# Kernel tuning notes

Hardware: AMD Instinct MI355X
Metric: run time of the kernel (lower is better)

The kernel has to match this reference:

```python
import jax, jax.numpy as jnp
import numpy as np

N = 65536      # samples
DX = 1024      # X features
DY = 1024      # Y features
D = 256        # projected width (x_net/y_net output)
LAMX = 0.1
LAMY = 0.1
SIGMA = 0.5    # STG gate noise std (eval-mode deterministic gate)
EPS = 0.001    # regularizer used in original code


def setup_inputs() -> dict:
    key = jax.random.key(0)
    ks = jax.random.split(key, 8)
    X = jax.random.normal(ks[0], (N, DX), dtype=jnp.float32)
    Y = jax.random.normal(ks[1], (N, DY), dtype=jnp.float32)
    # StochasticGates params (mu per input feature)
    mu_x = 0.01 * jax.random.normal(ks[2], (DX,), dtype=jnp.float32)
    mu_y = 0.01 * jax.random.normal(ks[3], (DY,), dtype=jnp.float32)
    # per-view linear nets (x_net: DX->D, y_net: DY->D)
    Wx = jax.random.normal(ks[4], (DX, D), dtype=jnp.float32) / np.sqrt(DX)
    bx = jnp.zeros((D,), dtype=jnp.float32)
    Wy = jax.random.normal(ks[5], (DY, D), dtype=jnp.float32) / np.sqrt(DY)
    by = jnp.zeros((D,), dtype=jnp.float32)
    return {"X": X, "Y": Y, "mu_x": mu_x, "mu_y": mu_y,
            "Wx": Wx, "bx": bx, "Wy": Wy, "by": by}


def _stg_gate(mu):
    # deterministic (eval) hard gate: clamp(mu + 0.5, 0, 1)
    return jnp.clip(mu + 0.5, 0.0, 1.0)


def _stg_reg(mu, lam):
    # lam * mean(P(gate > 0)) = lam * mean(Phi(mu/sigma))  [Gaussian CDF]
    return lam * jnp.mean(0.5 * (1.0 + jax.lax.erf(mu / (SIGMA * jnp.sqrt(2.0)))))


def _cov(a, b):
    # matches torch: (b.T @ a).T / (N-1) == a.T @ b / (N-1)
    n = a.shape[0]
    return (a.T @ b) / (n - 1)


def _inv_sqrt_sym(A):
    # A^(-1/2) via eigendecomposition; A symmetric so eigh == eig with V^-1 = V.T
    w, V = jnp.linalg.eigh(A)
    return (V * (w + EPS) ** (-0.5)) @ V.T


def _corr(Xh, Yh):
    d = Xh.shape[1]
    psi_x = Xh - Xh.mean(axis=0)
    psi_y = Yh - Yh.mean(axis=0)
    C_yy = _cov(psi_y, psi_y)
    C_yx = _cov(psi_y, psi_x)
    C_xy = _cov(psi_x, psi_y)
    C_xx = _cov(psi_x, psi_x)
    I = jnp.eye(d, dtype=Xh.dtype)
    C_yy_inv_root = _inv_sqrt_sym(C_yy + EPS * I)
    C_xx_inv = jnp.linalg.inv(C_xx + EPS * I)
    M = C_yy_inv_root @ C_yx @ C_xx_inv @ C_xy @ C_yy_inv_root
    return jnp.trace(M) / d


def reference(X, Y, mu_x, mu_y, Wx, bx, Wy, by):
    Xh = (X * _stg_gate(mu_x)) @ Wx + bx   # [N, D]
    Yh = (Y * _stg_gate(mu_y)) @ Wy + by   # [N, D]
    loss = -_corr(Xh, Yh) + _stg_reg(mu_x, LAMX) + _stg_reg(mu_y, LAMY)
    return loss
```

## Files before the change

kernel.cpp:

```cpp
#include <hip/hip_runtime.h>

#define N_S   65536
#define DXF   1024
#define DD    256
#define NM1   65535.0f
#define EPSR  0.001f

typedef __attribute__((ext_vector_type(4)))  float          f32x4;
typedef __attribute__((ext_vector_type(16))) float          f32x16;
typedef __attribute__((ext_vector_type(8)))  short          bf16x8;
typedef __attribute__((ext_vector_type(4)))  unsigned short ushort4_t;
typedef __attribute__((ext_vector_type(8)))  unsigned short ushort8_t;

__device__ __forceinline__ unsigned short f2bf(float f){
  unsigned u = __float_as_uint(f);
  u += 0x7fffu + ((u >> 16) & 1u);
  return (unsigned short)(u >> 16);
}
__device__ __forceinline__ float bf2f(unsigned short h){
  return __uint_as_float(((unsigned)h) << 16);
}
__device__ __forceinline__ f32x4 mfma16(bf16x8 a, bf16x8 b, f32x4 c){
  return __builtin_amdgcn_mfma_f32_16x16x32_bf16(a, b, c, 0, 0, 0);
}
__device__ __forceinline__ f32x16 mfma32(bf16x8 a, bf16x8 b, f32x16 c){
  return __builtin_amdgcn_mfma_f32_32x32x16_bf16(a, b, c, 0, 0, 0);
}
__device__ __forceinline__ void gld_lds16(const void* g, void* l){
  __builtin_amdgcn_global_load_lds(
      (const __attribute__((address_space(1))) unsigned int*)g,
      (__attribute__((address_space(3))) unsigned int*)l, 16, 0, 0);
}

#define VMCNT(N) asm volatile("s_waitcnt vmcnt(" #N ")" ::: "memory")

__global__ void k_prep(const float* __restrict__ Wx, const float* __restrict__ Wy,
                       const float* __restrict__ mux, const float* __restrict__ muy,
                       unsigned short* __restrict__ WTx, unsigned short* __restrict__ WTy,
                       float* __restrict__ scal){
  int v = blockIdx.y;
  const float* W  = v ? Wy  : Wx;
  const float* mu = v ? muy : mux;
  unsigned short* WT = v ? WTy : WTx;
  int j = threadIdx.x;
  if (j < 4){
    float ph = 0.5f * (1.f + erff(mu[blockIdx.x * 4 + j] * 1.41421356237f));
    atomicAdd(scal + 2 + v, 9.765625e-5f * ph);
  }
  #pragma unroll
  for (int r = 0; r < 4; ++r){
    int k = blockIdx.x * 4 + r;
    float g = fminf(fmaxf(mu[k] + 0.5f, 0.f), 1.f);
    WT[(size_t)(k >> 3) * 2048 + j * 8 + (k & 7)] = f2bf(g * W[(size_t)k * DD + j]);
  }
}

__global__ __launch_bounds__(512, 4) void k_gemm9(
    const float* __restrict__ X, const float* __restrict__ Y,
    const unsigned short* __restrict__ WTx, const unsigned short* __restrict__ WTy,
    unsigned short* __restrict__ Xhb, unsigned short* __restrict__ Yhb){
  const float* A = blockIdx.z ? Y : X;
  const unsigned short* WT = blockIdx.z ? WTy : WTx;
  unsigned short* Out = blockIdx.z ? Yhb : Xhb;

  __shared__ unsigned short As[2][64][136];

  int tid = threadIdx.x, lane = tid & 63, wid = tid >> 6;
  int row0 = blockIdx.x * 64;

  f32x4 acc[4][2] = {};

  int s_row = tid >> 3, s_f4 = tid & 7;
  const float* ap = A + (size_t)(row0 + s_row) * DXF + s_f4 * 4;

  const unsigned short* bB = WT + (size_t)(lane >> 4) * 2048
                           + (wid * 32 + (lane & 15)) * 8;

  float4 ar0, ar1, ar2, ar3;
  auto writeA = [&](int b){
    union { unsigned u[2]; ushort4_t v; } w;
    asm("v_cvt_pk_bf16_f32 %0, %1, %2" : "=v"(w.u[0]) : "v"(ar0.x), "v"(ar0.y));
    asm("v_cvt_pk_bf16_f32 %0, %1, %2" : "=v"(w.u[1]) : "v"(ar0.z), "v"(ar0.w));
    *(ushort4_t*)&As[b][s_row][s_f4 * 4] = w.v;
    asm("v_cvt_pk_bf16_f32 %0, %1, %2" : "=v"(w.u[0]) : "v"(ar1.x), "v"(ar1.y));
    asm("v_cvt_pk_bf16_f32 %0, %1, %2" : "=v"(w.u[1]) : "v"(ar1.z), "v"(ar1.w));
    *(ushort4_t*)&As[b][s_row][s_f4 * 4 + 32] = w.v;
    asm("v_cvt_pk_bf16_f32 %0, %1, %2" : "=v"(w.u[0]) : "v"(ar2.x), "v"(ar2.y));
    asm("v_cvt_pk_bf16_f32 %0, %1, %2" : "=v"(w.u[1]) : "v"(ar2.z), "v"(ar2.w));
    *(ushort4_t*)&As[b][s_row][s_f4 * 4 + 64] = w.v;
    asm("v_cvt_pk_bf16_f32 %0, %1, %2" : "=v"(w.u[0]) : "v"(ar3.x), "v"(ar3.y));
    asm("v_cvt_pk_bf16_f32 %0, %1, %2" : "=v"(w.u[1]) : "v"(ar3.z), "v"(ar3.w));
    *(ushort4_t*)&As[b][s_row][s_f4 * 4 + 96] = w.v;
  };
  auto loadA = [&](int kc){
    const float* p = ap + kc * 128;
    ar0 = *(const float4*)(p);
    ar1 = *(const float4*)(p + 32);
    ar2 = *(const float4*)(p + 64);
    ar3 = *(const float4*)(p + 96);
  };

  loadA(0);
  VMCNT(0);
  writeA(0);
  asm volatile("s_waitcnt lgkmcnt(0)" ::: "memory");
  __builtin_amdgcn_s_barrier();

#define GSTEP(S, BA, BB) { \
    bf16x8 af0 = *(const bf16x8*)&As[buf][     (lane & 15)][S * 32 + (lane >> 4) * 8]; \
    bf16x8 af1 = *(const bf16x8*)&As[buf][16 + (lane & 15)][S * 32 + (lane >> 4) * 8]; \
    bf16x8 af2 = *(const bf16x8*)&As[buf][32 + (lane & 15)][S * 32 + (lane >> 4) * 8]; \
    bf16x8 af3 = *(const bf16x8*)&As[buf][48 + (lane & 15)][S * 32 + (lane >> 4) * 8]; \
    acc[0][0] = mfma16(af0, BA, acc[0][0]); acc[0][1] = mfma16(af0, BB, acc[0][1]); \
    acc[1][0] = mfma16(af1, BA, acc[1][0]); acc[1][1] = mfma16(af1, BB, acc[1][1]); \
    acc[2][0] = mfma16(af2, BA, acc[2][0]); acc[2][1] = mfma16(af2, BB, acc[2][1]); \
    acc[3][0] = mfma16(af3, BA, acc[3][0]); acc[3][1] = mfma16(af3, BB, acc[3][1]); }

  #pragma unroll
  for (int c = 0; c < 8; ++c){
    int buf = c & 1;
    const unsigned short* bc = bB + c * 32768;
    bf16x8 b0a = *(const bf16x8*)(bc);
    bf16x8 b0b = *(const bf16x8*)(bc + 128);
    bf16x8 b1a = *(const bf16x8*)(bc + 8192);
    bf16x8 b1b = *(const bf16x8*)(bc + 8320);
    bf16x8 b2a = *(const bf16x8*)(bc + 16384);
    bf16x8 b2b = *(const bf16x8*)(bc + 16512);
    bf16x8 b3a = *(const bf16x8*)(bc + 24576);
    bf16x8 b3b = *(const bf16x8*)(bc + 24704);
    asm volatile("" ::: "memory");
    if (c < 7) loadA(c + 1);

    if (c < 7) { VMCNT(10); } else { VMCNT(6); }
    __builtin_amdgcn_sched_barrier(0);
    GSTEP(0, b0a, b0b)
    if (c < 7) { VMCNT(8); } else { VMCNT(4); }
    __builtin_amdgcn_sched_barrier(0);
    GSTEP(1, b1a, b1b)
    if (c < 7) { VMCNT(6); } else { VMCNT(2); }
    __builtin_amdgcn_sched_barrier(0);
    GSTEP(2, b2a, b2b)
    if (c < 7) { VMCNT(4); } else { VMCNT(0); }
    __builtin_amdgcn_sched_barrier(0);
    GSTEP(3, b3a, b3b)

    if (c < 7){
      VMCNT(0);
      __builtin_amdgcn_sched_barrier(0);
      writeA(buf ^ 1);
      asm volatile("s_waitcnt lgkmcnt(0)" ::: "memory");
      __builtin_amdgcn_s_barrier();
    }
  }
#undef GSTEP

  __syncthreads();
  unsigned short* tl = &As[0][0][0];
  #pragma unroll
  for (int r = 0; r < 4; ++r)
    #pragma unroll
    for (int t = 0; t < 2; ++t)
      #pragma unroll
      for (int rr = 0; rr < 4; ++rr){
        int row = r * 16 + (lane >> 4) * 4 + rr;
        int col = wid * 32 + t * 16 + (lane & 15);
        tl[row * 256 + col] = f2bf(acc[r][t][rr]);
      }
  __syncthreads();
  unsigned short* ob = Out + (size_t)row0 * DD;
  #pragma unroll
  for (int r = 0; r < 4; ++r){
    int off = r * 4096 + tid * 8;
    *(ushort8_t*)(ob + off) = *(const ushort8_t*)(tl + off);
  }
}

__global__ __launch_bounds__(512) void k_gram(
    const unsigned short* __restrict__ Xhb, const unsigned short* __restrict__ Yhb,
    float* __restrict__ part, float* __restrict__ sx, float* __restrict__ sy, int P){
  int type = blockIdx.z;
  int p = blockIdx.x;
  int chunk = N_S / P;
  int r0 = p * chunk;
  const unsigned short* Asrc = (type == 0) ? Xhb : Yhb;
  const unsigned short* Bsrc = (type == 1) ? Yhb : Xhb;
  bool dualB = (type == 2);

  __shared__ unsigned short At[256][40];
  __shared__ unsigned short Bt[256][40];

  int tid = threadIdx.x;
  int lane = tid & 63, wid = tid >> 6;
  int wr = wid >> 1, wc = wid & 1;

  f32x4 acc[4][8] = {};
  float cs0 = 0.f, cs1 = 0.f;

  int cp  = tid & 127;
  int kb0 = tid >> 7;

  unsigned ua[2][4], ub[2][4];

  auto loadT = [&](int ks){
    int base = r0 + ks * 32;
    #pragma unroll
    for (int r = 0; r < 2; ++r){
      int kb = kb0 + r * 4;
      #pragma unroll
      for (int kr = 0; kr < 4; ++kr){
        ua[r][kr] = *(const unsigned*)(Asrc + (size_t)(base + kb * 4 + kr) * DD + cp * 2);
        if (dualB)
          ub[r][kr] = *(const unsigned*)(Bsrc + (size_t)(base + kb * 4 + kr) * DD + cp * 2);
      }
    }
  };
  auto storeT = [&](){
    #pragma unroll
    for (int r = 0; r < 2; ++r){
      int kb = kb0 + r * 4;
      ushort4_t lo = { (unsigned short)ua[r][0], (unsigned short)ua[r][1],
                       (unsigned short)ua[r][2], (unsigned short)ua[r][3] };
      ushort4_t hi = { (unsigned short)(ua[r][0] >> 16), (unsigned short)(ua[r][1] >> 16),
                       (unsigned short)(ua[r][2] >> 16), (unsigned short)(ua[r][3] >> 16) };
      *(ushort4_t*)&At[cp * 2][kb * 4]     = lo;
      *(ushort4_t*)&At[cp * 2 + 1][kb * 4] = hi;
      if (type < 2){
        #pragma unroll
        for (int kr = 0; kr < 4; ++kr){
          cs0 += bf2f((unsigned short)ua[r][kr]);
          cs1 += bf2f((unsigned short)(ua[r][kr] >> 16));
        }
      }
      if (dualB){
        ushort4_t lob = { (unsigned short)ub[r][0], (unsigned short)ub[r][1],
                          (unsigned short)ub[r][2], (unsigned short)ub[r][3] };
        ushort4_t hib = { (unsigned short)(ub[r][0] >> 16), (unsigned short)(ub[r][1] >> 16),
                          (unsigned short)(ub[r][2] >> 16), (unsigned short)(ub[r][3] >> 16) };
        *(ushort4_t*)&Bt[cp * 2][kb * 4]     = lob;
        *(ushort4_t*)&Bt[cp * 2 + 1][kb * 4] = hib;
      }
    }
  };

  unsigned short (*Btp)[40] = dualB ? Bt : At;

  int KS = chunk / 32;
  loadT(0);
  for (int ks = 0; ks < KS; ++ks){
    __syncthreads();
    storeT();
    __syncthreads();
    if (ks + 1 < KS) loadT(ks + 1);
    bf16x8 af[4], bfv[8];
    #pragma unroll
    for (int mi = 0; mi < 4; ++mi)
      af[mi] = *(const bf16x8*)&At[wr * 64 + mi * 16 + (lane & 15)][(lane >> 4) * 8];
    #pragma unroll
    for (int ni = 0; ni < 8; ++ni)
      bfv[ni] = *(const bf16x8*)&Btp[wc * 128 + ni * 16 + (lane & 15)][(lane >> 4) * 8];
    #pragma unroll
    for (int mi = 0; mi < 4; ++mi)
      #pragma unroll
      for (int ni = 0; ni < 8; ++ni)
        acc[mi][ni] = mfma16(af[mi], bfv[ni], acc[mi][ni]);
  }

  float* dst = part + ((size_t)p * 3 + type) * 65536;
  #pragma unroll
  for (int mi = 0; mi < 4; ++mi)
    #pragma unroll
    for (int ni = 0; ni < 8; ++ni)
      #pragma unroll
      for (int rr = 0; rr < 4; ++rr){
        int grow = wr * 64 + mi * 16 + (lane >> 4) * 4 + rr;
        int gcol = wc * 128 + ni * 16 + (lane & 15);
        dst[(size_t)grow * 256 + gcol] = acc[mi][ni][rr];
      }

  if (type < 2){
    __syncthreads();
    float* red = (float*)&At[0][0];
    red[kb0 * 256 + cp * 2]     = cs0;
    red[kb0 * 256 + cp * 2 + 1] = cs1;
    __syncthreads();
    if (tid < 256){
      float s = red[tid] + red[256 + tid] + red[512 + tid] + red[768 + tid];
      atomicAdd((type == 0 ? sx : sy) + tid, s);
    }
  }
}

__global__ void k_reduce(const float* __restrict__ part, const float* __restrict__ sx,
                         const float* __restrict__ sy, float* __restrict__ Am,
                         float* __restrict__ Bm,
                         unsigned short* __restrict__ Abf, unsigned short* __restrict__ Bbf,
                         unsigned short* __restrict__ Cbf, unsigned short* __restrict__ CbfT,
                         float* __restrict__ scal, int P){
  __shared__ float r2[256];
  int i = blockIdx.x, j = threadIdx.x;
  size_t idx = (size_t)i * 256 + j;
  float gxx = 0.f, gyy = 0.f, gyx = 0.f;
  for (int p = 0; p < P; ++p){
    const float* b = part + (size_t)p * 3 * 65536;
    gxx += b[idx];
    gyy += b[65536 + idx];
    gyx += b[131072 + idx];
  }
  float invn1 = 1.f / NM1;
  float invn  = 1.f / (float)N_S;
  float sxi = sx[i], sxj = sx[j], syi = sy[i], syj = sy[j];
  float diag = (i == j) ? 1.f : 0.f;
  float am = (gyy - syi * syj * invn) * invn1 + diag * (2.f * EPSR);
  float bm = (gxx - sxi * sxj * invn) * invn1 + diag * EPSR;
  float cv = (gyx - syi * sxj * invn) * invn1;
  Am[idx] = am;  Bm[idx] = bm;
  Abf[idx] = f2bf(am);
  Bbf[idx] = f2bf(bm);
  Cbf[idx] = f2bf(cv);
  CbfT[(size_t)j * 256 + i] = f2bf(cv);
  r2[j] = fabsf(am);
  __syncthreads();
  for (int s = 128; s > 0; s >>= 1){ if (j < s) r2[j] += r2[j + s]; __syncthreads(); }
  if (j == 0) atomicMax((unsigned*)scal + 5, __float_as_uint(r2[0]));
  __syncthreads();
  r2[j] = fabsf(bm);
  __syncthreads();
  for (int s = 128; s > 0; s >>= 1){ if (j < s) r2[j] += r2[j + s]; __syncthreads(); }
  if (j == 0) atomicMax((unsigned*)scal + 6, __float_as_uint(r2[0]));
}

__global__ void k_x1(const float* __restrict__ Am, const float* __restrict__ Bm,
                     unsigned short* __restrict__ X0, const float* __restrict__ scal){
  int m = blockIdx.y;
  const unsigned* su = (const unsigned*)scal;
  float al = 1.9f / __uint_as_float(su[5 + m]);
  const float* M = m ? Bm : Am;
  int e = blockIdx.x * 512 + threadIdx.x;
  float v = -al * al * M[e];
  if ((e >> 8) == (e & 255)) v += 2.f * al;
  X0[m * 65536 + e] = f2bf(v);
}

__global__ __launch_bounds__(512) void k_it(
    const unsigned short* __restrict__ Abf, const unsigned short* __restrict__ Bbf,
    const unsigned short* __restrict__ Xc, unsigned short* __restrict__ Xn){
  int m = blockIdx.y, j = blockIdx.x;
  const unsigned short* M  = m ? Bbf : Abf;
  const unsigned short* Xm = Xc + m * 65536;
  unsigned short*       Xo = Xn + m * 65536;

  __shared__ unsigned short XJ[32 * 256];
  __shared__ unsigned short TT[32 * 256];

  int tid = threadIdx.x, lane = tid & 63, w = tid >> 6;
  int r31 = lane & 31, kh = lane >> 5;

  #pragma unroll
  for (int i = 0; i < 2; ++i){
    int rl = w * 4 + i * 2 + kh;
    int cg = ((lane & 31) - rl) & 31;
    gld_lds16(Xm + (size_t)(j * 32 + rl) * 256 + cg * 8, &XJ[(w * 4 + i * 2) * 256]);
  }
  asm volatile("s_waitcnt vmcnt(0)" ::: "memory");
  __builtin_amdgcn_s_barrier();

  f32x16 acc = {};
  const unsigned short* arow = M + (size_t)(w * 32 + r31) * 256 + kh * 8;
  #pragma unroll
  for (int ks = 0; ks < 16; ++ks){
    bf16x8 af = *(const bf16x8*)(arow + ks * 16);
    int ch = ((ks * 2 + kh) + r31) & 31;
    bf16x8 bf = *(const bf16x8*)&XJ[r31 * 256 + ch * 8];
    acc = mfma32(af, bf, acc);
  }
  #pragma unroll
  for (int reg = 0; reg < 16; ++reg){
    int kk = w * 32 + (reg & 3) + ((reg >> 2) << 3) + (kh << 2);
    int ch = ((kk >> 3) + r31) & 31;
    TT[r31 * 256 + ch * 8 + (kk & 7)] = f2bf(acc[reg]);
  }
  __syncthreads();

  f32x16 acc2 = {};
  const unsigned short* xrow = Xm + (size_t)(w * 32 + r31) * 256 + kh * 8;
  #pragma unroll
  for (int ks = 0; ks < 16; ++ks){
    bf16x8 af = *(const bf16x8*)(xrow + ks * 16);
    int ch = ((ks * 2 + kh) + r31) & 31;
    bf16x8 bf = *(const bf16x8*)&TT[r31 * 256 + ch * 8];
    acc2 = mfma32(af, bf, acc2);
  }
  #pragma unroll
  for (int reg = 0; reg < 16; ++reg){
    int row = w * 32 + (reg & 3) + ((reg >> 2) << 3) + (kh << 2);
    int ch = ((row >> 3) + r31) & 31;
    float xv = bf2f(XJ[r31 * 256 + ch * 8 + (row & 7)]);
    Xo[(size_t)row * 256 + j * 32 + r31] = f2bf(2.f * xv - acc2[reg]);
  }
}

__global__ __launch_bounds__(512) void k_uv(
    const unsigned short* __restrict__ Xf,
    const unsigned short* __restrict__ Cbf, const unsigned short* __restrict__ CbfT,
    float* __restrict__ U, float* __restrict__ W){
  int m = blockIdx.y, j = blockIdx.x;
  __shared__ unsigned short BJ[32 * 256];
  int tid = threadIdx.x, lane = tid & 63, w = tid >> 6;
  int r31 = lane & 31, kh = lane >> 5;
  const unsigned short* Brows = m ? (Xf + 65536) : CbfT;
  const unsigned short* Arows = m ? Cbf : Xf;
  float* D = m ? W : U;

  #pragma unroll
  for (int i = 0; i < 2; ++i){
    int rl = w * 4 + i * 2 + kh;
    int cg = ((lane & 31) - rl) & 31;
    gld_lds16(Brows + (size_t)(j * 32 + rl) * 256 + cg * 8, &BJ[(w * 4 + i * 2) * 256]);
  }
  asm volatile("s_waitcnt vmcnt(0)" ::: "memory");
  __builtin_amdgcn_s_barrier();

  f32x16 acc = {};
  const unsigned short* ar = Arows + (size_t)(w * 32 + r31) * 256 + kh * 8;
  #pragma unroll
  for (int ks = 0; ks < 16; ++ks){
    bf16x8 af = *(const bf16x8*)(ar + ks * 16);
    int ch = ((ks * 2 + kh) + r31) & 31;
    bf16x8 bf = *(const bf16x8*)&BJ[r31 * 256 + ch * 8];
    acc = mfma32(af, bf, acc);
  }
  #pragma unroll
  for (int reg = 0; reg < 16; ++reg){
    int row = w * 32 + (reg & 3) + ((reg >> 2) << 3) + (kh << 2);
    D[(size_t)row * 256 + j * 32 + r31] = acc[reg];
  }
}

__global__ __launch_bounds__(1024) void k_fin(const float* __restrict__ U,
                                              const float* __restrict__ W,
                                              const float* __restrict__ scal,
                                              float* __restrict__ out){
  __shared__ float red[1024];
  int tid = threadIdx.x;
  float t = 0.f;
  #pragma unroll
  for (int r = 0; r < 16; ++r){
    int i = r * 4096 + tid * 4;
    float4 u = *(const float4*)(U + i);
    float4 w = *(const float4*)(W + i);
    t += u.x * w.x + u.y * w.y + u.z * w.z + u.w * w.w;
  }
  red[tid] = t; __syncthreads();
  for (int s = 512; s > 0; s >>= 1){ if (tid < s) red[tid] += red[tid + s]; __syncthreads(); }
  if (tid == 0) out[0] = -red[0] / 256.f + scal[2] + scal[3];
}

extern "C" void kernel_launch(void* const* d_in, const int* in_sizes, int n_in,
                              void* d_out, int out_size, void* d_ws, size_t ws_size,
                              hipStream_t stream){
  (void)in_sizes; (void)n_in; (void)out_size;
  const float* X   = (const float*)d_in[0];
  const float* Y   = (const float*)d_in[1];
  const float* mux = (const float*)d_in[2];
  const float* muy = (const float*)d_in[3];
  const float* Wx  = (const float*)d_in[4];
  const float* Wy  = (const float*)d_in[6];
  float* out = (float*)d_out;
  char* ws = (char*)d_ws;

  const size_t MB = 1ull << 20;
  const size_t KB = 1024;
  size_t oXHB = 0;
  size_t oYHB = 32 * MB;
  size_t oWTX = 64 * MB;
  size_t oWTY = oWTX + 512 * KB;
  size_t oSX  = oWTY + 512 * KB;
  size_t oSY  = oSX + 4 * KB;
  size_t oSC  = oSY + 4 * KB;
  size_t oA   = oSC + 4 * KB;
  size_t oB   = oA   + 256 * KB;
  size_t oABF = oB   + 256 * KB;
  size_t oBBF = oABF + 128 * KB;
  size_t oCBF = oBBF + 128 * KB;
  size_t oCBT = oCBF + 128 * KB;
  size_t oX0  = oCBT + 128 * KB;
  size_t oX1  = oX0  + 256 * KB;
  size_t oTB  = oX1  + 256 * KB;
  size_t oU   = oTB  + 256 * KB;
  size_t oV   = oU   + 256 * KB;
  size_t oPart = 68 * MB;

  size_t per = 3ull * 65536 * 4;
  int P = 64;
  while (P > 8 && oPart + (size_t)P * per > ws_size) P >>= 1;

  unsigned short* Xhb = (unsigned short*)(ws + oXHB);
  unsigned short* Yhb = (unsigned short*)(ws + oYHB);
  unsigned short* WTx = (unsigned short*)(ws + oWTX);
  unsigned short* WTy = (unsigned short*)(ws + oWTY);
  float* sx   = (float*)(ws + oSX);
  float* sy   = (float*)(ws + oSY);
  float* scal = (float*)(ws + oSC);
  float* Am   = (float*)(ws + oA);
  float* Bm   = (float*)(ws + oB);
  unsigned short* Abf  = (unsigned short*)(ws + oABF);
  unsigned short* Bbf  = (unsigned short*)(ws + oBBF);
  unsigned short* Cbf  = (unsigned short*)(ws + oCBF);
  unsigned short* CbfT = (unsigned short*)(ws + oCBT);
  unsigned short* X0   = (unsigned short*)(ws + oX0);
  unsigned short* X1   = (unsigned short*)(ws + oX1);
  float* U    = (float*)(ws + oU);
  float* V    = (float*)(ws + oV);
  float* part = (float*)(ws + oPart);

  hipMemsetAsync(ws + oSX, 0, 12 * KB, stream);

  k_prep<<<dim3(256, 2), 256, 0, stream>>>(Wx, Wy, mux, muy, WTx, WTy, scal);
  k_gemm9<<<dim3(1024, 1, 2), 512, 0, stream>>>(X, Y, WTx, WTy, Xhb, Yhb);
  k_gram<<<dim3(P, 1, 3), 512, 0, stream>>>(Xhb, Yhb, part, sx, sy, P);
  k_reduce<<<256, 256, 0, stream>>>(part, sx, sy, Am, Bm, Abf, Bbf, Cbf, CbfT, scal, P);

  k_x1<<<dim3(128, 2), 512, 0, stream>>>(Am, Bm, X0, scal);
  k_it<<<dim3(8, 2), 512, 0, stream>>>(Abf, Bbf, X0, X1);
  k_it<<<dim3(8, 2), 512, 0, stream>>>(Abf, Bbf, X1, X0);
  k_it<<<dim3(8, 2), 512, 0, stream>>>(Abf, Bbf, X0, X1);
  k_it<<<dim3(8, 2), 512, 0, stream>>>(Abf, Bbf, X1, X0);
  k_it<<<dim3(8, 2), 512, 0, stream>>>(Abf, Bbf, X0, X1);
  k_uv<<<dim3(8, 2), 512, 0, stream>>>(X1, Cbf, CbfT, U, V);
  k_fin<<<1, 1024, 0, stream>>>(U, V, scal, out);
}
```

Before: 286.1 us.

## Use 2x4 warp tiling and XOR-swizzled LDS layout in projection GEMM

Changes the warp layout of the X/Y projection GEMM from 8 warps each owning a 64x32 column strip to a 2x4 warp grid where each warp owns a 32x64 tile. Each A fragment is now reused across four B fragments instead of two, which halves LDS A-fragment reads per MFMA, at the cost of twice as many B loads from global memory per warp. The LDS A tile drops its padding in favour of an XOR swizzle with 16-byte writes, meant to avoid bank conflicts. The kernel is heavily bound by streaming the fp32 inputs, so the main cost targeted is LDS traffic and instruction overhead.

Result: slower. 338.6 us (+18.4%).

```diff
diff --git a/kernel.cpp b/kernel.cpp
--- a/kernel.cpp
+++ b/kernel.cpp
@@ -55,7 +55,7 @@
   }
 }
 
-__global__ __launch_bounds__(512, 4) void k_gemm9(
+__global__ __launch_bounds__(512, 4) void k_gemm10(
     const float* __restrict__ X, const float* __restrict__ Y,
     const unsigned short* __restrict__ WTx, const unsigned short* __restrict__ WTy,
     unsigned short* __restrict__ Xhb, unsigned short* __restrict__ Yhb){
@@ -63,41 +63,44 @@
   const unsigned short* WT = blockIdx.z ? WTy : WTx;
   unsigned short* Out = blockIdx.z ? Yhb : Xhb;
 
-  __shared__ unsigned short As[2][64][136];
+  __shared__ unsigned short As[2][64][128];
 
   int tid = threadIdx.x, lane = tid & 63, wid = tid >> 6;
+  int wr = wid >> 2, wc = wid & 3;
   int row0 = blockIdx.x * 64;
 
-  f32x4 acc[4][2] = {};
-
-  int s_row = tid >> 3, s_f4 = tid & 7;
-  const float* ap = A + (size_t)(row0 + s_row) * DXF + s_f4 * 4;
+  f32x4 acc[2][4] = {};
+
+  int s_row = tid >> 3, s_p = tid & 7;
+  const float* ap = A + (size_t)(row0 + s_row) * DXF + s_p * 8;
 
   const unsigned short* bB = WT + (size_t)(lane >> 4) * 2048
-                           + (wid * 32 + (lane & 15)) * 8;
-
-  float4 ar0, ar1, ar2, ar3;
-  auto writeA = [&](int b){
-    union { unsigned u[2]; ushort4_t v; } w;
-    asm("v_cvt_pk_bf16_f32 %0, %1, %2" : "=v"(w.u[0]) : "v"(ar0.x), "v"(ar0.y));
-    asm("v_cvt_pk_bf16_f32 %0, %1, %2" : "=v"(w.u[1]) : "v"(ar0.z), "v"(ar0.w));
-    *(ushort4_t*)&As[b][s_row][s_f4 * 4] = w.v;
-    asm("v_cvt_pk_bf16_f32 %0, %1, %2" : "=v"(w.u[0]) : "v"(ar1.x), "v"(ar1.y));
-    asm("v_cvt_pk_bf16_f32 %0, %1, %2" : "=v"(w.u[1]) : "v"(ar1.z), "v"(ar1.w));
-    *(ushort4_t*)&As[b][s_row][s_f4 * 4 + 32] = w.v;
-    asm("v_cvt_pk_bf16_f32 %0, %1, %2" : "=v"(w.u[0]) : "v"(ar2.x), "v"(ar2.y));
-    asm("v_cvt_pk_bf16_f32 %0, %1, %2" : "=v"(w.u[1]) : "v"(ar2.z), "v"(ar2.w));
-    *(ushort4_t*)&As[b][s_row][s_f4 * 4 + 64] = w.v;
-    asm("v_cvt_pk_bf16_f32 %0, %1, %2" : "=v"(w.u[0]) : "v"(ar3.x), "v"(ar3.y));
-    asm("v_cvt_pk_bf16_f32 %0, %1, %2" : "=v"(w.u[1]) : "v"(ar3.z), "v"(ar3.w));
-    *(ushort4_t*)&As[b][s_row][s_f4 * 4 + 96] = w.v;
-  };
+                           + (wc * 64 + (lane & 15)) * 8;
+
+  float4 a0, a1, a2, a3;
   auto loadA = [&](int kc){
     const float* p = ap + kc * 128;
-    ar0 = *(const float4*)(p);
-    ar1 = *(const float4*)(p + 32);
-    ar2 = *(const float4*)(p + 64);
-    ar3 = *(const float4*)(p + 96);
+    a0 = *(const float4*)(p);
+    a1 = *(const float4*)(p + 4);
+    a2 = *(const float4*)(p + 64);
+    a3 = *(const float4*)(p + 68);
+  };
+  auto writeA = [&](int b){
+    union { unsigned u[4]; ushort8_t v; } w;
+    asm("v_cvt_pk_bf16_f32 %0, %1, %2" : "=v"(w.u[0]) : "v"(a0.x), "v"(a0.y));
+    asm("v_cvt_pk_bf16_f32 %0, %1, %2" : "=v"(w.u[1]) : "v"(a0.z), "v"(a0.w));
+    asm("v_cvt_pk_bf16_f32 %0, %1, %2" : "=v"(w.u[2]) : "v"(a1.x), "v"(a1.y));
+    asm("v_cvt_pk_bf16_f32 %0, %1, %2" : "=v"(w.u[3]) : "v"(a1.z), "v"(a1.w));
+    *(ushort8_t*)&As[b][s_row][(s_p ^ (s_row & 15)) * 8] = w.v;
+    asm("v_cvt_pk_bf16_f32 %0, %1, %2" : "=v"(w.u[0]) : "v"(a2.x), "v"(a2.y));
+    asm("v_cvt_pk_bf16_f32 %0, %1, %2" : "=v"(w.u[1]) : "v"(a2.z), "v"(a2.w));
+    asm("v_cvt_pk_bf16_f32 %0, %1, %2" : "=v"(w.u[2]) : "v"(a3.x), "v"(a3.y));
+    asm("v_cvt_pk_bf16_f32 %0, %1, %2" : "=v"(w.u[3]) : "v"(a3.z), "v"(a3.w));
+    *(ushort8_t*)&As[b][s_row][((s_p + 8) ^ (s_row & 15)) * 8] = w.v;
+  };
+  auto afrag = [&](int buf, int S, int mi) -> bf16x8 {
+    int s = (S * 4 + (lane >> 4)) ^ (lane & 15);
+    return *(const bf16x8*)&As[buf][wr * 32 + mi * 16 + (lane & 15)][s * 8];
   };
 
   loadA(0);
@@ -106,43 +109,49 @@
   asm volatile("s_waitcnt lgkmcnt(0)" ::: "memory");
   __builtin_amdgcn_s_barrier();
 
-#define GSTEP(S, BA, BB) { \
-    bf16x8 af0 = *(const bf16x8*)&As[buf][     (lane & 15)][S * 32 + (lane >> 4) * 8]; \
-    bf16x8 af1 = *(const bf16x8*)&As[buf][16 + (lane & 15)][S * 32 + (lane >> 4) * 8]; \
-    bf16x8 af2 = *(const bf16x8*)&As[buf][32 + (lane & 15)][S * 32 + (lane >> 4) * 8]; \
-    bf16x8 af3 = *(const bf16x8*)&As[buf][48 + (lane & 15)][S * 32 + (lane >> 4) * 8]; \
-    acc[0][0] = mfma16(af0, BA, acc[0][0]); acc[0][1] = mfma16(af0, BB, acc[0][1]); \
-    acc[1][0] = mfma16(af1, BA, acc[1][0]); acc[1][1] = mfma16(af1, BB, acc[1][1]); \
-    acc[2][0] = mfma16(af2, BA, acc[2][0]); acc[2][1] = mfma16(af2, BB, acc[2][1]); \
-    acc[3][0] = mfma16(af3, BA, acc[3][0]); acc[3][1] = mfma16(af3, BB, acc[3][1]); }
+#define GSTEP(S, B0, B1, B2, B3) { \
+    bf16x8 af0 = afrag(buf, S, 0); \
+    bf16x8 af1 = afrag(buf, S, 1); \
+    acc[0][0] = mfma16(af0, B0, acc[0][0]); acc[1][0] = mfma16(af1, B0, acc[1][0]); \
+    acc[0][1] = mfma16(af0, B1, acc[0][1]); acc[1][1] = mfma16(af1, B1, acc[1][1]); \
+    acc[0][2] = mfma16(af0, B2, acc[0][2]); acc[1][2] = mfma16(af1, B2, acc[1][2]); \
+    acc[0][3] = mfma16(af0, B3, acc[0][3]); acc[1][3] = mfma16(af1, B3, acc[1][3]); }
 
   #pragma unroll
   for (int c = 0; c < 8; ++c){
     int buf = c & 1;
     const unsigned short* bc = bB + c * 32768;
-    bf16x8 b0a = *(const bf16x8*)(bc);
-    bf16x8 b0b = *(const bf16x8*)(bc + 128);
-    bf16x8 b1a = *(const bf16x8*)(bc + 8192);
-    bf16x8 b1b = *(const bf16x8*)(bc + 8320);
-    bf16x8 b2a = *(const bf16x8*)(bc + 16384);
-    bf16x8 b2b = *(const bf16x8*)(bc + 16512);
-    bf16x8 b3a = *(const bf16x8*)(bc + 24576);
-    bf16x8 b3b = *(const bf16x8*)(bc + 24704);
+    bf16x8 b00 = *(const bf16x8*)(bc);
+    bf16x8 b01 = *(const bf16x8*)(bc + 128);
+    bf16x8 b02 = *(const bf16x8*)(bc + 256);
+    bf16x8 b03 = *(const bf16x8*)(bc + 384);
+    bf16x8 b10 = *(const bf16x8*)(bc + 8192);
+    bf16x8 b11 = *(const bf16x8*)(bc + 8320);
+    bf16x8 b12 = *(const bf16x8*)(bc + 8448);
+    bf16x8 b13 = *(const bf16x8*)(bc + 8576);
+    bf16x8 b20 = *(const bf16x8*)(bc + 16384);
+    bf16x8 b21 = *(const bf16x8*)(bc + 16512);
+    bf16x8 b22 = *(const bf16x8*)(bc + 16640);
+    bf16x8 b23 = *(const bf16x8*)(bc + 16768);
+    bf16x8 b30 = *(const bf16x8*)(bc + 24576);
+    bf16x8 b31 = *(const bf16x8*)(bc + 24704);
+    bf16x8 b32 = *(const bf16x8*)(bc + 24832);
+    bf16x8 b33 = *(const bf16x8*)(bc + 24960);
     asm volatile("" ::: "memory");
     if (c < 7) loadA(c + 1);
 
-    if (c < 7) { VMCNT(10); } else { VMCNT(6); }
+    if (c < 7) { VMCNT(16); } else { VMCNT(12); }
     __builtin_amdgcn_sched_barrier(0);
-    GSTEP(0, b0a, b0b)
+    GSTEP(0, b00, b01, b02, b03)
+    if (c < 7) { VMCNT(12); } else { VMCNT(8); }
+    __builtin_amdgcn_sched_barrier(0);
+    GSTEP(1, b10, b11, b12, b13)
     if (c < 7) { VMCNT(8); } else { VMCNT(4); }
     __builtin_amdgcn_sched_barrier(0);
-    GSTEP(1, b1a, b1b)
-    if (c < 7) { VMCNT(6); } else { VMCNT(2); }
-    __builtin_amdgcn_sched_barrier(0);
-    GSTEP(2, b2a, b2b)
+    GSTEP(2, b20, b21, b22, b23)
     if (c < 7) { VMCNT(4); } else { VMCNT(0); }
     __builtin_amdgcn_sched_barrier(0);
-    GSTEP(3, b3a, b3b)
+    GSTEP(3, b30, b31, b32, b33)
 
     if (c < 7){
       VMCNT(0);
@@ -157,14 +166,14 @@
   __syncthreads();
   unsigned short* tl = &As[0][0][0];
   #pragma unroll
-  for (int r = 0; r < 4; ++r)
-    #pragma unroll
-    for (int t = 0; t < 2; ++t)
+  for (int mi = 0; mi < 2; ++mi)
+    #pragma unroll
+    for (int ni = 0; ni < 4; ++ni)
       #pragma unroll
       for (int rr = 0; rr < 4; ++rr){
-        int row = r * 16 + (lane >> 4) * 4 + rr;
-        int col = wid * 32 + t * 16 + (lane & 15);
-        tl[row * 256 + col] = f2bf(acc[r][t][rr]);
+        int row = wr * 32 + mi * 16 + (lane >> 4) * 4 + rr;
+        int col = wc * 64 + ni * 16 + (lane & 15);
+        tl[row * 256 + col] = f2bf(acc[mi][ni][rr]);
       }
   __syncthreads();
   unsigned short* ob = Out + (size_t)row0 * DD;
@@ -516,7 +525,7 @@
   hipMemsetAsync(ws + oSX, 0, 12 * KB, stream);
 
   k_prep<<<dim3(256, 2), 256, 0, stream>>>(Wx, Wy, mux, muy, WTx, WTy, scal);
-  k_gemm9<<<dim3(1024, 1, 2), 512, 0, stream>>>(X, Y, WTx, WTy, Xhb, Yhb);
+  k_gemm10<<<dim3(1024, 1, 2), 512, 0, stream>>>(X, Y, WTx, WTy, Xhb, Yhb);
   k_gram<<<dim3(P, 1, 3), 512, 0, stream>>>(Xhb, Yhb, part, sx, sy, P);
   k_reduce<<<256, 256, 0, stream>>>(part, sx, sy, Am, Bm, Abf, Bbf, Cbf, CbfT, scal, P);
 
```
